# Kernel tuning notes

Measured on AMD Instinct MI355X. Metric: run time of the kernel, lower is better.

The kernel has to match this reference:

```python
import jax, jax.numpy as jnp
import numpy as np

B, S, H, L = 64, 512, 768, 2
OP, C, M, E, A = 18, 24, 16, 8, 3
K = C + M + E          # 48 operand classes
PAD = 0                # label_pad_id


def _linear(x, W, b):
    return x @ W.T + b


def _ln(x, g, b):
    mu = x.mean(-1, keepdims=True)
    v = ((x - mu) ** 2).mean(-1, keepdims=True)
    return (x - mu) / jnp.sqrt(v + 1e-5) * g + b


def _proj(x, W, b, g, be):
    return _ln(_linear(x, W, b), g, be)


def _mlp(x, W1, b1, W2, b2):
    return _linear(jax.nn.relu(_linear(x, W1, b1)), W2, b2)


def _gru(x, hx, Wih, Whh, bih, bhh):
    # single time-step multi-layer GRU (torch nn.GRU gate math), x:[B,H], hx:[L,B,H]
    hs = []
    for l in range(L):
        gi = _linear(x, Wih[l], bih[l])
        gh = _linear(hx[l], Whh[l], bhh[l])
        ir, iz, inn = jnp.split(gi, 3, axis=-1)
        hr, hz, hn = jnp.split(gh, 3, axis=-1)
        r = jax.nn.sigmoid(ir + hr)
        z = jax.nn.sigmoid(iz + hz)
        n = jnp.tanh(inn + r * hn)
        x = (1.0 - z) * n + z * hx[l]
        hs.append(x)
    return x, jnp.stack(hs)


def _pick(idx, pc, pn, prev, bidx):
    # get_operand_vector: const -> projected const, number -> projected number, else previous result
    is_c = idx < C
    i2 = idx - C
    is_n = (i2 >= 0) & (i2 < M)
    i3 = i2 - M
    is_p = (i3 >= 0) & (i3 < E)
    v = jnp.where(is_c[:, None], pc[jnp.clip(idx, 0, C - 1)], 0.0)
    v = jnp.where(is_n[:, None], pn[bidx, jnp.clip(i2, 0, M - 1)], v)
    v = jnp.where(is_p[:, None], prev[bidx, jnp.clip(i3, 0, E - 1)], v)
    return v


def _forward(inp, const_vector, operator_vector, opj_W, opj_b, opj_g, opj_be, odj_W, odj_b, odj_g, odj_be, opc_W1, opc_b1, opc_W2, opc_b2, odc_W1, odc_b1, odc_W2, odc_b2, og_Wih, og_Whh, og_bih, og_bhh, cg_Wih, cg_Whh, cg_bih, cg_bhh, number_mask, gold_operators, gold_operands):
    Bv, Sv, Hv = inp.shape
    # _get_num_vec (concat=True): first/last token embedding per number id
    match = number_mask[:, :, None] == (jnp.arange(M) + 1)[None, None, :]   # [B,S,M]
    exists = match.any(axis=1)                                              # [B,M]
    first = jnp.argmax(match, axis=1)
    last = Sv - 1 - jnp.argmax(match[:, ::-1, :], axis=1)
    fv = jnp.take_along_axis(inp, first[..., None], axis=1)                 # [B,M,H]
    lv = jnp.take_along_axis(inp, last[..., None], axis=1)
    num_vec = jnp.where(exists[..., None], jnp.concatenate([fv, lv], -1), 0.0)  # [B,M,2H]
    pn = _proj(num_vec, odj_W, odj_b, odj_g, odj_be)                        # [B,M,H]
    pc = _proj(const_vector, odj_W, odj_b, odj_g, odj_be)                   # [C,H]
    gold_opv = _proj(operator_vector[gold_operators], opj_W, opj_b, opj_g, opj_be)  # [B,E,H]

    prev = jnp.zeros((Bv, E, Hv), inp.dtype)   # previous_result_vector
    bidx = jnp.arange(Bv)
    cv = inp[:, 0, :]
    ctx_hx = None
    op_logits, od_logits = [], []
    for i in range(E):
        if i > 0:
            cv, _ = _gru(cv, ctx_hx, cg_Wih, cg_Whh, cg_bih, cg_bhh)
        op_logits.append(_mlp(cv, opc_W1, opc_b1, opc_W2, opc_b2))
        hx = jnp.broadcast_to(cv, (L, Bv, Hv))
        step_logits = []
        pred = None
        for j in range(A):
            if j == 0:
                x = gold_opv[:, i]  # teacher forcing (module default training=True)
            else:
                x = _pick(gold_operands[:, i, j - 1], pc, pn, prev, bidx)
            x, hx = _gru(x, hx, og_Wih, og_Whh, og_bih, og_bhh)
            logit = _mlp(x, odc_W1, odc_b1, odc_W2, odc_b2)
            step_logits.append(logit)
            oidx = jnp.argmax(logit, axis=1)
            empty = jnp.max(prev[:, i, :], axis=-1) == 0
            cond = (oidx < C) & (oidx == PAD) & empty
            prev = prev.at[:, i].set(jnp.where(cond[:, None], x, prev[:, i]))
            pred = _pick(oidx, pc, pn, prev, bidx)
        empty = jnp.max(prev[:, i, :], axis=-1) == 0
        prev = prev.at[:, i].set(jnp.where(empty[:, None], pred, prev[:, i]))
        ctx_hx = jnp.broadcast_to(prev[:, i], (L, Bv, Hv))
        od_logits.append(jnp.stack(step_logits, axis=1))
    return jnp.stack(op_logits, axis=1), jnp.stack(od_logits, axis=1)


def setup_inputs() -> dict:
    key = jax.random.key(0)
    ks = iter(jax.random.split(key, 48))
    def rn(shape, s=0.02):
        return jax.random.normal(next(ks), shape, jnp.float32) * s
    d = {}
    d["input"] = jax.random.normal(next(ks), (B, S, H), jnp.float32)
    d["attention_mask"] = jax.random.randint(next(ks), (B, S), 0, 2, jnp.int32)
    d["question_mask"] = jax.random.randint(next(ks), (B, S), 0, 2, jnp.int32)
    d["number_mask"] = jax.random.randint(next(ks), (B, S), 0, M + 1, jnp.int32)
    d["gold_operators"] = jax.random.randint(next(ks), (B, E), 0, OP, jnp.int32)
    d["gold_operands"] = jax.random.randint(next(ks), (B, E, A), 0, K, jnp.int32)
    d["const_vector"] = rn((C, 2 * H), 1.0)
    d["operator_vector"] = rn((OP, 2 * H), 1.0)
    d["opj_W"] = rn((H, 2 * H)); d["opj_b"] = jnp.zeros(H); d["opj_g"] = jnp.ones(H); d["opj_be"] = jnp.zeros(H)
    d["odj_W"] = rn((H, 2 * H)); d["odj_b"] = jnp.zeros(H); d["odj_g"] = jnp.ones(H); d["odj_be"] = jnp.zeros(H)
    d["opc_W1"] = rn((H // 2, H)); d["opc_b1"] = jnp.zeros(H // 2)
    d["opc_W2"] = rn((OP, H // 2)); d["opc_b2"] = jnp.zeros(OP)
    d["odc_W1"] = rn((K // 2, H)); d["odc_b1"] = jnp.zeros(K // 2)
    d["odc_W2"] = rn((K, K // 2)); d["odc_b2"] = jnp.zeros(K)
    for p in ["og", "cg"]:
        d[p + "_Wih"] = rn((L, 3 * H, H)); d[p + "_Whh"] = rn((L, 3 * H, H))
        d[p + "_bih"] = jnp.zeros((L, 3 * H)); d[p + "_bhh"] = jnp.zeros((L, 3 * H))
    return d


def reference(input, attention_mask, question_mask, number_mask, gold_operators, gold_operands, const_vector, operator_vector, opj_W, opj_b, opj_g, opj_be, odj_W, odj_b, odj_g, odj_be, opc_W1, opc_b1, opc_W2, opc_b2, odc_W1, odc_b1, odc_W2, odc_b2, og_Wih, og_Whh, og_bih, og_bhh, cg_Wih, cg_Whh, cg_bih, cg_bhh):
    # attention_mask / question_mask are unused by the original forward as well
    return _forward(input, const_vector, operator_vector, opj_W, opj_b, opj_g, opj_be, odj_W, odj_b, odj_g, odj_be, opc_W1, opc_b1, opc_W2, opc_b2, odc_W1, odc_b1, odc_W2, odc_b2, og_Wih, og_Whh, og_bih, og_bhh, cg_Wih, cg_Whh, cg_bih, cg_bhh, number_mask, gold_operators, gold_operands)
```

## Files before the change

kernel.cpp:

```cpp
#include <hip/hip_runtime.h>
#include <math.h>

constexpr int B_  = 64;
constexpr int S_  = 512;
constexpr int H_  = 768;
constexpr int H2_ = 1536;
constexpr int G3_ = 2304;
constexpr int OP_ = 18;
constexpr int C_  = 24;
constexpr int M_  = 16;
constexpr int E_  = 8;
constexpr int A_  = 3;
constexpr int K_  = 48;
constexpr int HH_ = 384;

using f32x4  = __attribute__((ext_vector_type(4))) float;
using short8 = __attribute__((ext_vector_type(8))) short;

#define MFMA16(a, b, c) __builtin_amdgcn_mfma_f32_16x16x32_bf16((a), (b), (c), 0, 0, 0)

__device__ __forceinline__ void split1(float x, short& h, short& l)
{
    union { float f; unsigned u; } a; a.f = x;
    h = (short)(a.u >> 16);
    union { unsigned u; float f; } hb; hb.u = a.u & 0xffff0000u;
    union { float f; unsigned u; } r; r.f = x - hb.f;
    l = (short)(r.u >> 16);
}

__device__ __forceinline__ void cvt8(float4 p0, float4 p1, short8& hi, short8& lo)
{
    float x[8] = {p0.x, p0.y, p0.z, p0.w, p1.x, p1.y, p1.z, p1.w};
    #pragma unroll
    for (int e = 0; e < 8; ++e) { short h, l; split1(x[e], h, l); hi[e] = h; lo[e] = l; }
}

__global__ void k_split_all(
    const float* __restrict__ s0, short* __restrict__ h0, short* __restrict__ l0, int e0,
    const float* __restrict__ s1, short* __restrict__ h1, short* __restrict__ l1, int e1,
    const float* __restrict__ s2, short* __restrict__ h2, short* __restrict__ l2, int e2,
    const float* __restrict__ s3, short* __restrict__ h3, short* __restrict__ l3, int e3,
    const float* __restrict__ s4, short* __restrict__ h4, short* __restrict__ l4, int e4,
    const float* __restrict__ s5, short* __restrict__ h5, short* __restrict__ l5, int e5)
{
    int t = blockIdx.x * 256 + threadIdx.x;
    if (t >= e5) return;
    const float* src; short* hi; short* lo; int base;
    if      (t < e0) { src = s0; hi = h0; lo = l0; base = 0;  }
    else if (t < e1) { src = s1; hi = h1; lo = l1; base = e0; }
    else if (t < e2) { src = s2; hi = h2; lo = l2; base = e1; }
    else if (t < e3) { src = s3; hi = h3; lo = l3; base = e2; }
    else if (t < e4) { src = s4; hi = h4; lo = l4; base = e3; }
    else             { src = s5; hi = h5; lo = l5; base = e4; }
    int u = t - base;
    float4 v = ((const float4*)src)[u];
    float x[4] = {v.x, v.y, v.z, v.w};
    short h[4], l[4];
    #pragma unroll
    for (int e = 0; e < 4; ++e) split1(x[e], h[e], l[e]);
    ((short4*)hi)[u] = make_short4(h[0], h[1], h[2], h[3]);
    ((short4*)lo)[u] = make_short4(l[0], l[1], l[2], l[3]);
}

__global__ __launch_bounds__(512) void k_gru_mfma(
    int ghonly,
    const short* __restrict__ xhi, const short* __restrict__ xlo, long ldx, int pickmode,
    const int* __restrict__ gopd, int i, int jm1,
    const short* __restrict__ pchi, const short* __restrict__ pclo,
    const short* __restrict__ pnhi, const short* __restrict__ pnlo,
    const short* __restrict__ pvhi, const short* __restrict__ pvlo,
    const short* __restrict__ hhi, const short* __restrict__ hlo, long ldh,
    const short* __restrict__ Wih_hi, const short* __restrict__ Wih_lo,
    const short* __restrict__ Whh_hi, const short* __restrict__ Whh_lo,
    float* __restrict__ C)
{
    const int tid  = threadIdx.x;
    const int lane = tid & 63;
    const int w    = tid >> 6;
    const int bx   = blockIdx.x;
    const bool hside = ghonly || (bx >= 72);
    const int n0 = ((hside && !ghonly) ? bx - 72 : bx) * 32;
    const int koff = (lane >> 4) * 8;

    const short* ahi[4]; const short* alo[4];
    #pragma unroll
    for (int rt = 0; rt < 4; ++rt) {
        int r = rt * 16 + (lane & 15);
        long off;
        const short *bh_, *bl_;
        if (hside) { bh_ = hhi; bl_ = hlo; off = (long)r * ldh; }
        else if (!pickmode) { bh_ = xhi; bl_ = xlo; off = (long)r * ldx; }
        else {
            int idx = gopd[(r * E_ + i) * A_ + jm1];
            if (idx < C_)           { bh_ = pchi; bl_ = pclo; off = (long)idx * H_; }
            else if (idx < C_ + M_) { bh_ = pnhi; bl_ = pnlo; off = ((long)r * M_ + (idx - C_)) * H_; }
            else                    { bh_ = pvhi; bl_ = pvlo; off = ((long)r * E_ + (idx - C_ - M_)) * H_; }
        }
        ahi[rt] = bh_ + off + koff;
        alo[rt] = bl_ + off + koff;
    }
    const short* whi[2]; const short* wlo[2];
    const short* WH = hside ? Whh_hi : Wih_hi;
    const short* WL = hside ? Whh_lo : Wih_lo;
    #pragma unroll
    for (int nt = 0; nt < 2; ++nt) {
        long off = (long)(n0 + nt * 16 + (lane & 15)) * H_ + koff;
        whi[nt] = WH + off;
        wlo[nt] = WL + off;
    }

    f32x4 acc[4][2];
    #pragma unroll
    for (int rt = 0; rt < 4; ++rt)
        #pragma unroll
        for (int nt = 0; nt < 2; ++nt) acc[rt][nt] = (f32x4){0.f, 0.f, 0.f, 0.f};

    for (int kt = w * 3; kt < w * 3 + 3; ++kt) {
        const int kb = kt * 32;
        short8 Ah[4], Al[4];
        #pragma unroll
        for (int rt = 0; rt < 4; ++rt) {
            Ah[rt] = *(const short8*)(ahi[rt] + kb);
            Al[rt] = *(const short8*)(alo[rt] + kb);
        }
        #pragma unroll
        for (int nt = 0; nt < 2; ++nt) {
            short8 Bh = *(const short8*)(whi[nt] + kb);
            short8 Bl = *(const short8*)(wlo[nt] + kb);
            #pragma unroll
            for (int rt = 0; rt < 4; ++rt) {
                acc[rt][nt] = MFMA16(Ah[rt], Bh, acc[rt][nt]);
                acc[rt][nt] = MFMA16(Ah[rt], Bl, acc[rt][nt]);
                acc[rt][nt] = MFMA16(Al[rt], Bh, acc[rt][nt]);
            }
        }
    }

    __shared__ f32x4 Lr[8][8][64];
    #pragma unroll
    for (int rt = 0; rt < 4; ++rt)
        #pragma unroll
        for (int nt = 0; nt < 2; ++nt)
            Lr[w][rt * 2 + nt][lane] = acc[rt][nt];
    __syncthreads();
    {
        const int f  = w;
        const int rt = f >> 1, nt = f & 1;
        f32x4 s = Lr[0][f][lane];
        #pragma unroll
        for (int q = 1; q < 8; ++q) s = s + Lr[q][f][lane];
        float* Cb = C + (hside ? 2304 : 0) + n0;
        int col = nt * 16 + (lane & 15);
        int rb  = rt * 16 + ((lane >> 4) << 2);
        #pragma unroll
        for (int r = 0; r < 4; ++r)
            Cb[(long)(rb + r) * 4608 + col] = s[r];
    }
}

__global__ __launch_bounds__(512) void k_gi_pre(
    const short* __restrict__ xhi, const short* __restrict__ xlo,
    const short* __restrict__ Whi, const short* __restrict__ Wlo,
    float* __restrict__ C)
{
    const int tid  = threadIdx.x;
    const int lane = tid & 63;
    const int w    = tid >> 6;
    const int n0 = blockIdx.x * 32;
    const int r0 = blockIdx.y * 64;
    const int koff = (lane >> 4) * 8;

    const short* ahi[4]; const short* alo[4];
    #pragma unroll
    for (int rt = 0; rt < 4; ++rt) {
        long off = (long)(r0 + rt * 16 + (lane & 15)) * H_ + koff;
        ahi[rt] = xhi + off;
        alo[rt] = xlo + off;
    }
    const short* whi[2]; const short* wlo[2];
    #pragma unroll
    for (int nt = 0; nt < 2; ++nt) {
        long off = (long)(n0 + nt * 16 + (lane & 15)) * H_ + koff;
        whi[nt] = Whi + off;
        wlo[nt] = Wlo + off;
    }

    f32x4 acc[4][2];
    #pragma unroll
    for (int rt = 0; rt < 4; ++rt)
        #pragma unroll
        for (int nt = 0; nt < 2; ++nt) acc[rt][nt] = (f32x4){0.f, 0.f, 0.f, 0.f};

    for (int kt = w * 3; kt < w * 3 + 3; ++kt) {
        const int kb = kt * 32;
        short8 Ah[4], Al[4];
        #pragma unroll
        for (int rt = 0; rt < 4; ++rt) {
            Ah[rt] = *(const short8*)(ahi[rt] + kb);
            Al[rt] = *(const short8*)(alo[rt] + kb);
        }
        #pragma unroll
        for (int nt = 0; nt < 2; ++nt) {
            short8 Bh = *(const short8*)(whi[nt] + kb);
            short8 Bl = *(const short8*)(wlo[nt] + kb);
            #pragma unroll
            for (int rt = 0; rt < 4; ++rt) {
                acc[rt][nt] = MFMA16(Ah[rt], Bh, acc[rt][nt]);
                acc[rt][nt] = MFMA16(Ah[rt], Bl, acc[rt][nt]);
                acc[rt][nt] = MFMA16(Al[rt], Bh, acc[rt][nt]);
            }
        }
    }

    __shared__ f32x4 Lr[8][8][64];
    #pragma unroll
    for (int rt = 0; rt < 4; ++rt)
        #pragma unroll
        for (int nt = 0; nt < 2; ++nt)
            Lr[w][rt * 2 + nt][lane] = acc[rt][nt];
    __syncthreads();
    {
        const int f  = w;
        const int rt = f >> 1, nt = f & 1;
        f32x4 s = Lr[0][f][lane];
        #pragma unroll
        for (int q = 1; q < 8; ++q) s = s + Lr[q][f][lane];
        int col = n0 + nt * 16 + (lane & 15);
        int rb  = r0 + rt * 16 + ((lane >> 4) << 2);
        #pragma unroll
        for (int r = 0; r < 4; ++r)
            C[(long)(rb + r) * G3_ + col] = s[r];
    }
}

__global__ __launch_bounds__(512) void k_proj_mfma(
    const float* __restrict__ Ab, long lda, const int* __restrict__ gidx, int Mm,
    const short* __restrict__ Whi, const short* __restrict__ Wlo, int wld,
    float* __restrict__ C, int ldc)
{
    const int tid  = threadIdx.x;
    const int lane = tid & 63;
    const int w    = tid >> 6;
    const int n0 = blockIdx.x * 64;
    const int r0 = blockIdx.y * 64;
    const int koff = (lane >> 4) * 8;

    const float* arow[4];
    #pragma unroll
    for (int rt = 0; rt < 4; ++rt) {
        int r = r0 + rt * 16 + (lane & 15);
        int rr = r < Mm ? r : (Mm - 1);
        const float* s = gidx ? (Ab + (long)gidx[rr] * lda) : (Ab + (long)rr * lda);
        arow[rt] = s + koff;
    }
    const short* whi[4]; const short* wlo[4];
    #pragma unroll
    for (int nt = 0; nt < 4; ++nt) {
        long off = (long)(n0 + nt * 16 + (lane & 15)) * wld + koff;
        whi[nt] = Whi + off; wlo[nt] = Wlo + off;
    }

    f32x4 acc[4][4];
    #pragma unroll
    for (int rt = 0; rt < 4; ++rt)
        #pragma unroll
        for (int nt = 0; nt < 4; ++nt) acc[rt][nt] = (f32x4){0.f, 0.f, 0.f, 0.f};

    for (int kt = w * 6; kt < w * 6 + 6; ++kt) {
        const int kb = kt * 32;
        short8 ah[4], al[4];
        #pragma unroll
        for (int rt = 0; rt < 4; ++rt) {
            float4 p0 = *(const float4*)(arow[rt] + kb);
            float4 p1 = *(const float4*)(arow[rt] + kb + 4);
            cvt8(p0, p1, ah[rt], al[rt]);
        }
        #pragma unroll
        for (int nt = 0; nt < 4; ++nt) {
            short8 Bh = *(const short8*)(whi[nt] + kb);
            short8 Bl = *(const short8*)(wlo[nt] + kb);
            #pragma unroll
            for (int rt = 0; rt < 4; ++rt) {
                acc[rt][nt] = MFMA16(ah[rt], Bh, acc[rt][nt]);
                acc[rt][nt] = MFMA16(ah[rt], Bl, acc[rt][nt]);
                acc[rt][nt] = MFMA16(al[rt], Bh, acc[rt][nt]);
            }
        }
    }

    __shared__ f32x4 Lr[112][64];
    if (w > 0) {
        #pragma unroll
        for (int rt = 0; rt < 4; ++rt)
            #pragma unroll
            for (int nt = 0; nt < 4; ++nt)
                Lr[(w - 1) * 16 + rt * 4 + nt][lane] = acc[rt][nt];
    }
    __syncthreads();
    if (w == 0) {
        #pragma unroll
        for (int rt = 0; rt < 4; ++rt)
            #pragma unroll
            for (int nt = 0; nt < 4; ++nt) {
                int f = rt * 4 + nt;
                f32x4 s = acc[rt][nt];
                #pragma unroll
                for (int q = 0; q < 7; ++q) s = s + Lr[q * 16 + f][lane];
                int col = n0 + nt * 16 + (lane & 15);
                int rb  = r0 + rt * 16 + ((lane >> 4) << 2);
                #pragma unroll
                for (int r = 0; r < 4; ++r)
                    if (rb + r < Mm) C[(long)(rb + r) * ldc + col] = s[r];
            }
    }
}

__global__ void k_gates2(const float* __restrict__ GI, long ldgi,
                         const float* __restrict__ GH, long ldgh,
                         const float* __restrict__ h, long ldh,
                         const float* __restrict__ bih, const float* __restrict__ bhh,
                         float* __restrict__ hnew,
                         short* __restrict__ hnhi, short* __restrict__ hnlo)
{
    int t = blockIdx.x * 256 + threadIdx.x;
    int b = t / 768, c = t - b * 768;
    const float* gi = GI + (long)b * ldgi;
    const float* gh = GH + (long)b * ldgh;
    float ir  = gi[c]        + bih[c];
    float iz  = gi[768 + c]  + bih[768 + c];
    float in_ = gi[1536 + c] + bih[1536 + c];
    float hr  = gh[c]        + bhh[c];
    float hz  = gh[768 + c]  + bhh[768 + c];
    float hn  = gh[1536 + c] + bhh[1536 + c];
    float r  = 1.f / (1.f + expf(-(ir + hr)));
    float z_ = 1.f / (1.f + expf(-(iz + hz)));
    float n  = tanhf(in_ + r * hn);
    float hp = h[(long)b * ldh + c];
    float v = (1.f - z_) * n + z_ * hp;
    hnew[t] = v;
    short sh, sl; split1(v, sh, sl);
    hnhi[t] = sh; hnlo[t] = sl;
}

__global__ void k_ln2(float* __restrict__ X, const float* __restrict__ bias,
                      const float* __restrict__ g, const float* __restrict__ be,
                      short* __restrict__ Xhi, short* __restrict__ Xlo)
{
    int row = blockIdx.x, tid = threadIdx.x;
    __shared__ float red[256];
    float* xr = X + (long)row * 768;
    float v[3];
    #pragma unroll
    for (int it = 0; it < 3; ++it) {
        int c2 = tid + it * 256;
        v[it] = xr[c2] + bias[c2];
    }
    float s = v[0] + v[1] + v[2];
    red[tid] = s; __syncthreads();
    for (int o = 128; o > 0; o >>= 1) { if (tid < o) red[tid] += red[tid + o]; __syncthreads(); }
    float mu = red[0] / 768.f;
    __syncthreads();
    float vv = 0.f;
    #pragma unroll
    for (int it = 0; it < 3; ++it) { float d = v[it] - mu; vv += d * d; }
    red[tid] = vv; __syncthreads();
    for (int o = 128; o > 0; o >>= 1) { if (tid < o) red[tid] += red[tid + o]; __syncthreads(); }
    float inv = 1.f / sqrtf(red[0] / 768.f + 1e-5f);
    #pragma unroll
    for (int it = 0; it < 3; ++it) {
        int c2 = tid + it * 256;
        float o2 = (v[it] - mu) * inv * g[c2] + be[c2];
        xr[c2] = o2;
        short sh, sl; split1(o2, sh, sl);
        Xhi[(long)row * 768 + c2] = sh;
        Xlo[(long)row * 768 + c2] = sl;
    }
}

__global__ __launch_bounds__(256) void k_ophead_fused(
    int do_gates,
    const float* __restrict__ GI,
    const float* __restrict__ bihg, const float* __restrict__ bhhg,
    const float* __restrict__ hp, long ldhp,
    float* __restrict__ cvf, short* __restrict__ cvhi, short* __restrict__ cvlo,
    const float* __restrict__ W1, const float* __restrict__ b1,
    const float* __restrict__ W2, const float* __restrict__ b2,
    float* __restrict__ op_out, int i)
{
    int b = blockIdx.x, tid = threadIdx.x;
    __shared__ float xs[768];
    __shared__ float hs[384];

    if (do_gates) {
        const float* gb = GI + (long)b * 4608;
        #pragma unroll
        for (int it = 0; it < 3; ++it) {
            int c2 = tid + it * 256;
            float ir  = gb[c2]        + bihg[c2];
            float iz  = gb[768 + c2]  + bihg[768 + c2];
            float in_ = gb[1536 + c2] + bihg[1536 + c2];
            float hr  = gb[2304 + c2] + bhhg[c2];
            float hz  = gb[3072 + c2] + bhhg[768 + c2];
            float hn  = gb[3840 + c2] + bhhg[1536 + c2];
            float r  = 1.f / (1.f + expf(-(ir + hr)));
            float z_ = 1.f / (1.f + expf(-(iz + hz)));
            float n  = tanhf(in_ + r * hn);
            float hpv = hp[(long)b * ldhp + c2];
            float v = (1.f - z_) * n + z_ * hpv;
            xs[c2] = v;
            cvf[(long)b * 768 + c2] = v;
            short sh, sl; split1(v, sh, sl);
            cvhi[(long)b * 768 + c2] = sh;
            cvlo[(long)b * 768 + c2] = sl;
        }
    } else {
        const float* xr = cvf + (long)b * 768;
        #pragma unroll
        for (int it = 0; it < 3; ++it) xs[tid + it * 256] = xr[tid + it * 256];
    }
    __syncthreads();

    for (int c = tid; c < 384; c += 256) {
        const float* wr = W1 + (long)c * 768;
        float acc = 0.f;
        #pragma unroll 8
        for (int k = 0; k < 768; k += 4) {
            float4 xv = *(const float4*)&xs[k];
            float4 wv = *(const float4*)(wr + k);
            acc += xv.x * wv.x + xv.y * wv.y + xv.z * wv.z + xv.w * wv.w;
        }
        hs[c] = fmaxf(acc + b1[c], 0.f);
    }
    __syncthreads();

    int c = tid >> 3, g = tid & 7;
    float acc = 0.f;
    if (c < OP_) {
        const float* wr = W2 + (long)c * HH_;
        #pragma unroll
        for (int t = 0; t < 12; ++t) {
            int k = (g + 8 * t) * 4;
            float4 xv = *(const float4*)&hs[k];
            float4 wv = *(const float4*)(wr + k);
            acc += xv.x * wv.x + xv.y * wv.y + xv.z * wv.z + xv.w * wv.w;
        }
    }
    acc += __shfl_xor(acc, 1);
    acc += __shfl_xor(acc, 2);
    acc += __shfl_xor(acc, 4);
    if (c < OP_ && g == 0)
        op_out[((long)b * E_ + i) * OP_ + c] = acc + b2[c];
}

__global__ __launch_bounds__(256) void k_odhead(
    const float* __restrict__ GI,
    const float* __restrict__ bihg, const float* __restrict__ bhhg,
    const float* __restrict__ hp, long ldhp,
    float* __restrict__ hx1f, short* __restrict__ hx1hi, short* __restrict__ hx1lo,
    const float* __restrict__ W1, const float* __restrict__ b1,
    const float* __restrict__ W2, const float* __restrict__ b2,
    float* __restrict__ od_base, long ldl,
    float* __restrict__ prev, int i,
    const float* __restrict__ pcb, const float* __restrict__ pnb,
    short* __restrict__ pvhi, short* __restrict__ pvlo,
    int do_final)
{
    int b = blockIdx.x, tid = threadIdx.x;
    __shared__ float xs[768];
    __shared__ float ps[768];
    __shared__ float hidL[24];
    __shared__ float lg[48];
    __shared__ float red[256];
    __shared__ int s_oidx;

    {
        const float* gb = GI + (long)b * 4608;
        #pragma unroll
        for (int it = 0; it < 3; ++it) {
            int c2 = tid + it * 256;
            float ir  = gb[c2]        + bihg[c2];
            float iz  = gb[768 + c2]  + bihg[768 + c2];
            float in_ = gb[1536 + c2] + bihg[1536 + c2];
            float hr  = gb[2304 + c2] + bhhg[c2];
            float hz  = gb[3072 + c2] + bhhg[768 + c2];
            float hn  = gb[3840 + c2] + bhhg[1536 + c2];
            float r  = 1.f / (1.f + expf(-(ir + hr)));
            float z_ = 1.f / (1.f + expf(-(iz + hz)));
            float n  = tanhf(in_ + r * hn);
            float hpv = hp[(long)b * ldhp + c2];
            float v = (1.f - z_) * n + z_ * hpv;
            xs[c2] = v;
            hx1f[(long)b * 768 + c2] = v;
            short sh, sl; split1(v, sh, sl);
            hx1hi[(long)b * 768 + c2] = sh;
            hx1lo[(long)b * 768 + c2] = sl;
        }
    }
    __syncthreads();

    int c = tid >> 3, g = tid & 7;
    float acc = 0.f;
    if (c < 24) {
        const float* wr = W1 + (long)c * 768;
        #pragma unroll
        for (int t = 0; t < 24; ++t) {
            int k = (g + 8 * t) * 4;
            float4 xv = *(const float4*)&xs[k];
            float4 wv = *(const float4*)(wr + k);
            acc += xv.x * wv.x + xv.y * wv.y + xv.z * wv.z + xv.w * wv.w;
        }
    }
    acc += __shfl_xor(acc, 1);
    acc += __shfl_xor(acc, 2);
    acc += __shfl_xor(acc, 4);
    if (c < 24 && g == 0) hidL[c] = fmaxf(acc + b1[c], 0.f);
    __syncthreads();

    if (tid < 48) {
        float a2 = b2[tid];
        const float* w2 = W2 + tid * 24;
        #pragma unroll
        for (int k = 0; k < 24; ++k) a2 += hidL[k] * w2[k];
        lg[tid] = a2;
        od_base[(long)b * ldl + tid] = a2;
    }

    long poff = ((long)b * E_ + i) * 768;
    float* prow = prev + poff;
    float m = -3.4e38f;
    #pragma unroll
    for (int it = 0; it < 3; ++it) m = fmaxf(m, prow[tid + it * 256]);
    red[tid] = m; __syncthreads();
    for (int o = 128; o > 0; o >>= 1) { if (tid < o) red[tid] = fmaxf(red[tid], red[tid + o]); __syncthreads(); }
    float m0 = red[0];

    if (tid == 0) {
        float best = lg[0]; int bi = 0;
        for (int k2 = 1; k2 < K_; ++k2) { float v = lg[k2]; if (v > best) { best = v; bi = k2; } }
        s_oidx = bi;
    }
    __syncthreads();
    int oidx = s_oidx;
    bool empty0 = (m0 == 0.0f);
    bool cond = (oidx == 0) && empty0;
    if (cond) {
        #pragma unroll
        for (int it = 0; it < 3; ++it) {
            int c2 = tid + it * 256;
            float v = xs[c2];
            prow[c2] = v;
            short sh, sl; split1(v, sh, sl);
            pvhi[poff + c2] = sh; pvlo[poff + c2] = sl;
        }
    }
    __syncthreads();

    if (!do_final) return;

    float mfin;
    if (cond) {
        float mx = -3.4e38f;
        #pragma unroll
        for (int it = 0; it < 3; ++it) mx = fmaxf(mx, xs[tid + it * 256]);
        red[tid] = mx; __syncthreads();
        for (int o = 128; o > 0; o >>= 1) { if (tid < o) red[tid] = fmaxf(red[tid], red[tid + o]); __syncthreads(); }
        mfin = red[0];
    } else {
        mfin = m0;
    }

    const float* src;
    if (oidx < C_)            src = pcb + (long)oidx * 768;
    else if (oidx < C_ + M_)  src = pnb + ((long)b * M_ + (oidx - C_)) * 768;
    else                      src = prev + ((long)b * E_ + (oidx - C_ - M_)) * 768;
    #pragma unroll
    for (int it = 0; it < 3; ++it) ps[tid + it * 256] = src[tid + it * 256];
    __syncthreads();

    if (mfin == 0.0f) {
        #pragma unroll
        for (int it = 0; it < 3; ++it) {
            int c2 = tid + it * 256;
            float v = ps[c2];
            prow[c2] = v;
            short sh, sl; split1(v, sh, sl);
            pvhi[poff + c2] = sh; pvlo[poff + c2] = sl;
        }
    }
}

__global__ void k_numvec(const float* __restrict__ inp, const int* __restrict__ nmask,
                         float* __restrict__ numvec)
{
    int b = blockIdx.x / M_, m = blockIdx.x % M_;
    int tid = threadIdx.x;
    int fmin = S_, lmax = -1;
    for (int s = tid; s < S_; s += 256) {
        if (nmask[b * S_ + s] == m + 1) {
            if (s < fmin) fmin = s;
            if (s > lmax) lmax = s;
        }
    }
    __shared__ int sf[256], sl[256];
    sf[tid] = fmin; sl[tid] = lmax; __syncthreads();
    for (int o = 128; o > 0; o >>= 1) {
        if (tid < o) {
            sf[tid] = min(sf[tid], sf[tid + o]);
            sl[tid] = max(sl[tid], sl[tid + o]);
        }
        __syncthreads();
    }
    int first = sf[0], last = sl[0];
    bool exists = (last >= 0);
    if (!exists) { first = 0; last = 0; }
    const float* fv = inp + ((long)b * S_ + first) * H_;
    const float* lv = inp + ((long)b * S_ + last) * H_;
    float* dst = numvec + ((long)b * M_ + m) * H2_;
    for (int h = tid; h < H_; h += 256) {
        dst[h]      = exists ? fv[h] : 0.f;
        dst[H_ + h] = exists ? lv[h] : 0.f;
    }
}

__global__ void k_copy_cv(const float* __restrict__ inp, float* __restrict__ cvv,
                          short* __restrict__ cvhi, short* __restrict__ cvlo)
{
    int b = blockIdx.x;
    for (int h = threadIdx.x; h < H_; h += 256) {
        float v = inp[(long)b * S_ * H_ + h];
        cvv[b * H_ + h] = v;
        short sh, sl; split1(v, sh, sl);
        cvhi[b * H_ + h] = sh; cvlo[b * H_ + h] = sl;
    }
}

extern "C" void kernel_launch(void* const* d_in, const int* in_sizes, int n_in,
                              void* d_out, int out_size, void* d_ws, size_t ws_size,
                              hipStream_t stream)
{
    const float* inp    = (const float*)d_in[0];
    const int*   nmask  = (const int*)  d_in[3];
    const int*   gops   = (const int*)  d_in[4];
    const int*   gopd   = (const int*)  d_in[5];
    const float* constv = (const float*)d_in[6];
    const float* opv    = (const float*)d_in[7];
    const float* opj_W  = (const float*)d_in[8];
    const float* opj_b  = (const float*)d_in[9];
    const float* opj_g  = (const float*)d_in[10];
    const float* opj_be = (const float*)d_in[11];
    const float* odj_W  = (const float*)d_in[12];
    const float* odj_b  = (const float*)d_in[13];
    const float* odj_g  = (const float*)d_in[14];
    const float* odj_be = (const float*)d_in[15];
    const float* opc_W1 = (const float*)d_in[16];
    const float* opc_b1 = (const float*)d_in[17];
    const float* opc_W2 = (const float*)d_in[18];
    const float* opc_b2 = (const float*)d_in[19];
    const float* odc_W1 = (const float*)d_in[20];
    const float* odc_b1 = (const float*)d_in[21];
    const float* odc_W2 = (const float*)d_in[22];
    const float* odc_b2 = (const float*)d_in[23];
    const float* og_Wih = (const float*)d_in[24];
    const float* og_Whh = (const float*)d_in[25];
    const float* og_bih = (const float*)d_in[26];
    const float* og_bhh = (const float*)d_in[27];
    const float* cg_Wih = (const float*)d_in[28];
    const float* cg_Whh = (const float*)d_in[29];
    const float* cg_bih = (const float*)d_in[30];
    const float* cg_bhh = (const float*)d_in[31];

    float* op_out = (float*)d_out;
    float* od_out = op_out + (long)B_ * E_ * OP_;

    float* ws      = (float*)d_ws;
    float* num_vec = ws; ws += (long)B_ * M_ * H2_;
    float* pn      = ws; ws += (long)B_ * M_ * H_;
    float* pcb     = ws; ws += (long)64 * H_;
    float* gopv    = ws; ws += (long)B_ * E_ * H_;
    float* prev    = ws; ws += (long)B_ * E_ * H_;
    float* gigh    = ws; ws += (long)B_ * 4608;
    float* gi_pre  = ws; ws += (long)B_ * E_ * G3_;
    float* cv      = ws; ws += (long)B_ * H_;
    float* h0      = ws; ws += (long)B_ * H_;
    float* hx0     = ws; ws += (long)B_ * H_;
    float* hx1     = ws; ws += (long)B_ * H_;

    auto alloc_s = [&](long elems) -> short* {
        short* p = (short*)ws; ws += elems / 2; return p;
    };
    const long nOG = (long)2 * G3_ * H_;
    short* og_ih_hi = alloc_s(nOG); short* og_ih_lo = alloc_s(nOG);
    short* og_hh_hi = alloc_s(nOG); short* og_hh_lo = alloc_s(nOG);
    short* cg_ih_hi = alloc_s(nOG); short* cg_ih_lo = alloc_s(nOG);
    short* cg_hh_hi = alloc_s(nOG); short* cg_hh_lo = alloc_s(nOG);
    const long nPJ = (long)H_ * H2_;
    short* odj_hi = alloc_s(nPJ); short* odj_lo = alloc_s(nPJ);
    short* opj_hi = alloc_s(nPJ); short* opj_lo = alloc_s(nPJ);
    short* pn_hi  = alloc_s((long)B_ * M_ * H_); short* pn_lo  = alloc_s((long)B_ * M_ * H_);
    short* pc_hi  = alloc_s((long)64 * H_);      short* pc_lo  = alloc_s((long)64 * H_);
    short* gv_hi  = alloc_s((long)B_ * E_ * H_); short* gv_lo  = alloc_s((long)B_ * E_ * H_);
    short* pv_hi  = alloc_s((long)B_ * E_ * H_); short* pv_lo  = alloc_s((long)B_ * E_ * H_);
    short* cv_hi  = alloc_s((long)B_ * H_);      short* cv_lo  = alloc_s((long)B_ * H_);
    short* h0_hi  = alloc_s((long)B_ * H_);      short* h0_lo  = alloc_s((long)B_ * H_);
    short* hx0_hi = alloc_s((long)B_ * H_);      short* hx0_lo = alloc_s((long)B_ * H_);
    short* hx1_hi = alloc_s((long)B_ * H_);      short* hx1_lo = alloc_s((long)B_ * H_);

    hipMemsetAsync(prev, 0, (size_t)B_ * E_ * H_ * sizeof(float), stream);
    hipMemsetAsync(pv_hi, 0, (size_t)2 * B_ * E_ * H_ * sizeof(short), stream);

    {
        int nOG4 = (int)(nOG / 4), nPJ4 = (int)(nPJ / 4);
        int e0 = nOG4, e1 = 2 * nOG4, e2 = 3 * nOG4, e3 = 4 * nOG4;
        int e4 = e3 + nPJ4, e5 = e4 + nPJ4;
        k_split_all<<<(e5 + 255) / 256, 256, 0, stream>>>(
            og_Wih, og_ih_hi, og_ih_lo, e0,
            og_Whh, og_hh_hi, og_hh_lo, e1,
            cg_Wih, cg_ih_hi, cg_ih_lo, e2,
            cg_Whh, cg_hh_hi, cg_hh_lo, e3,
            odj_W,  odj_hi,  odj_lo,  e4,
            opj_W,  opj_hi,  opj_lo,  e5);
    }

    k_numvec<<<B_ * M_, 256, 0, stream>>>(inp, nmask, num_vec);

    k_proj_mfma<<<dim3(12, 16), 512, 0, stream>>>(num_vec, H2_, nullptr, 1024,
                                                  odj_hi, odj_lo, H2_, pn, H_);
    k_ln2<<<1024, 256, 0, stream>>>(pn, odj_b, odj_g, odj_be, pn_hi, pn_lo);

    k_proj_mfma<<<dim3(12, 1), 512, 0, stream>>>(constv, H2_, nullptr, C_,
                                                 odj_hi, odj_lo, H2_, pcb, H_);
    k_ln2<<<C_, 256, 0, stream>>>(pcb, odj_b, odj_g, odj_be, pc_hi, pc_lo);

    k_proj_mfma<<<dim3(12, 8), 512, 0, stream>>>(opv, H2_, gops, 512,
                                                 opj_hi, opj_lo, H2_, gopv, H_);
    k_ln2<<<512, 256, 0, stream>>>(gopv, opj_b, opj_g, opj_be, gv_hi, gv_lo);

    k_gi_pre<<<dim3(72, 8), 512, 0, stream>>>(gv_hi, gv_lo, og_ih_hi, og_ih_lo, gi_pre);

    k_copy_cv<<<B_, 256, 0, stream>>>(inp, cv, cv_hi, cv_lo);

    const long ldE = (long)E_ * H_;
    const long lW  = (long)G3_ * H_;

    for (int i = 0; i < E_; ++i) {
        if (i > 0) {
            const float* hrow = prev + (long)(i - 1) * H_;
            const short* hrhi = pv_hi + (long)(i - 1) * H_;
            const short* hrlo = pv_lo + (long)(i - 1) * H_;
            k_gru_mfma<<<144, 512, 0, stream>>>(0, cv_hi, cv_lo, H_, 0, nullptr, 0, 0,
                                                nullptr, nullptr, nullptr, nullptr, nullptr, nullptr,
                                                hrhi, hrlo, ldE,
                                                cg_ih_hi, cg_ih_lo, cg_hh_hi, cg_hh_lo, gigh);
            k_gates2<<<192, 256, 0, stream>>>(gigh, 4608, gigh + 2304, 4608,
                                              hrow, ldE, cg_bih, cg_bhh, h0, h0_hi, h0_lo);
            k_gru_mfma<<<144, 512, 0, stream>>>(0, h0_hi, h0_lo, H_, 0, nullptr, 0, 0,
                                                nullptr, nullptr, nullptr, nullptr, nullptr, nullptr,
                                                hrhi, hrlo, ldE,
                                                cg_ih_hi + lW, cg_ih_lo + lW,
                                                cg_hh_hi + lW, cg_hh_lo + lW, gigh);
            k_ophead_fused<<<B_, 256, 0, stream>>>(1, gigh, cg_bih + G3_, cg_bhh + G3_,
                                                   hrow, ldE, cv, cv_hi, cv_lo,
                                                   opc_W1, opc_b1, opc_W2, opc_b2, op_out, i);
        } else {
            k_ophead_fused<<<B_, 256, 0, stream>>>(0, gigh, cg_bih, cg_bhh,
                                                   cv, H_, cv, cv_hi, cv_lo,
                                                   opc_W1, opc_b1, opc_W2, opc_b2, op_out, i);
        }

        for (int j = 0; j < A_; ++j) {
            const float* hp0 = (j == 0) ? cv : hx0;
            const float* hp1 = (j == 0) ? cv : hx1;
            const short* hp0hi = (j == 0) ? cv_hi : hx0_hi;
            const short* hp0lo = (j == 0) ? cv_lo : hx0_lo;
            const short* hp1hi = (j == 0) ? cv_hi : hx1_hi;
            const short* hp1lo = (j == 0) ? cv_lo : hx1_lo;

            if (j == 0) {
                k_gru_mfma<<<72, 512, 0, stream>>>(1, nullptr, nullptr, 0, 0, nullptr, 0, 0,
                                                   nullptr, nullptr, nullptr, nullptr, nullptr, nullptr,
                                                   hp0hi, hp0lo, H_,
                                                   og_ih_hi, og_ih_lo, og_hh_hi, og_hh_lo, gigh);
                k_gates2<<<192, 256, 0, stream>>>(gi_pre + (long)i * G3_, (long)E_ * G3_,
                                                  gigh + 2304, 4608,
                                                  hp0, H_, og_bih, og_bhh, hx0, hx0_hi, hx0_lo);
            } else {
                k_gru_mfma<<<144, 512, 0, stream>>>(0, nullptr, nullptr, 0, 1, gopd, i, j - 1,
                                                    pc_hi, pc_lo, pn_hi, pn_lo, pv_hi, pv_lo,
                                                    hp0hi, hp0lo, H_,
                                                    og_ih_hi, og_ih_lo, og_hh_hi, og_hh_lo, gigh);
                k_gates2<<<192, 256, 0, stream>>>(gigh, 4608, gigh + 2304, 4608,
                                                  hp0, H_, og_bih, og_bhh, hx0, hx0_hi, hx0_lo);
            }
            k_gru_mfma<<<144, 512, 0, stream>>>(0, hx0_hi, hx0_lo, H_, 0, nullptr, 0, 0,
                                                nullptr, nullptr, nullptr, nullptr, nullptr, nullptr,
                                                hp1hi, hp1lo, H_,
                                                og_ih_hi + lW, og_ih_lo + lW,
                                                og_hh_hi + lW, og_hh_lo + lW, gigh);

            float* od_base = od_out + ((long)i * A_ + j) * K_;
            k_odhead<<<B_, 256, 0, stream>>>(gigh, og_bih + G3_, og_bhh + G3_,
                                             hp1, H_, hx1, hx1_hi, hx1_lo,
                                             odc_W1, odc_b1, odc_W2, odc_b2,
                                             od_base, (long)E_ * A_ * K_,
                                             prev, i, pcb, pn, pv_hi, pv_lo,
                                             (j == A_ - 1) ? 1 : 0);
        }
    }
}
```

Baseline: 1.395 ms.

## Split GRU GEMM K dimension across two blocks with partial sums reduced in consumers

The per-step GRU matvec kernel now uses 256-thread blocks and a second grid dimension that splits the K=768 reduction in half. Each half writes its partials to a separate slab of the doubled gigh buffer. The gate kernels (k_gates2, ophead, odhead) add the two partials before applying the biases. This doubles the number of blocks to fill more of the GPU's compute units on these small latency-bound launches. The cost is extra global writes and reads of the partial sums and a slightly different float summation order.

Result: no change. 1.413 ms (+1.3%).

```diff
diff --git a/kernel.cpp b/kernel.cpp
--- a/kernel.cpp
+++ b/kernel.cpp
@@ -13,6 +13,7 @@
 constexpr int A_  = 3;
 constexpr int K_  = 48;
 constexpr int HH_ = 384;
+constexpr long HOFF = 294912;
 
 using f32x4  = __attribute__((ext_vector_type(4))) float;
 using short8 = __attribute__((ext_vector_type(8))) short;
@@ -62,7 +63,7 @@
     ((short4*)lo)[u] = make_short4(l[0], l[1], l[2], l[3]);
 }
 
-__global__ __launch_bounds__(512) void k_gru_mfma(
+__global__ __launch_bounds__(256) void k_gru_mfma(
     int ghonly,
     const short* __restrict__ xhi, const short* __restrict__ xlo, long ldx, int pickmode,
     const int* __restrict__ gopd, int i, int jm1,
@@ -78,6 +79,7 @@
     const int lane = tid & 63;
     const int w    = tid >> 6;
     const int bx   = blockIdx.x;
+    const int kz   = blockIdx.y;
     const bool hside = ghonly || (bx >= 72);
     const int n0 = ((hside && !ghonly) ? bx - 72 : bx) * 32;
     const int koff = (lane >> 4) * 8;
@@ -115,7 +117,8 @@
         #pragma unroll
         for (int nt = 0; nt < 2; ++nt) acc[rt][nt] = (f32x4){0.f, 0.f, 0.f, 0.f};
 
-    for (int kt = w * 3; kt < w * 3 + 3; ++kt) {
+    const int kt0 = kz * 12 + w * 3;
+    for (int kt = kt0; kt < kt0 + 3; ++kt) {
         const int kb = kt * 32;
         short8 Ah[4], Al[4];
         #pragma unroll
@@ -136,20 +139,21 @@
         }
     }
 
-    __shared__ f32x4 Lr[8][8][64];
+    __shared__ f32x4 Lr[4][8][64];
     #pragma unroll
     for (int rt = 0; rt < 4; ++rt)
         #pragma unroll
         for (int nt = 0; nt < 2; ++nt)
             Lr[w][rt * 2 + nt][lane] = acc[rt][nt];
     __syncthreads();
-    {
-        const int f  = w;
+    #pragma unroll
+    for (int ff = 0; ff < 2; ++ff) {
+        const int f  = w * 2 + ff;
         const int rt = f >> 1, nt = f & 1;
         f32x4 s = Lr[0][f][lane];
         #pragma unroll
-        for (int q = 1; q < 8; ++q) s = s + Lr[q][f][lane];
-        float* Cb = C + (hside ? 2304 : 0) + n0;
+        for (int q = 1; q < 4; ++q) s = s + Lr[q][f][lane];
+        float* Cb = C + (long)kz * HOFF + (hside ? 2304 : 0) + n0;
         int col = nt * 16 + (lane & 15);
         int rb  = rt * 16 + ((lane >> 4) << 2);
         #pragma unroll
@@ -315,8 +319,8 @@
     }
 }
 
-__global__ void k_gates2(const float* __restrict__ GI, long ldgi,
-                         const float* __restrict__ GH, long ldgh,
+__global__ void k_gates2(const float* __restrict__ GI, long ldgi, long gi2off,
+                         const float* __restrict__ GH, long ldgh, long gh2off,
                          const float* __restrict__ h, long ldh,
                          const float* __restrict__ bih, const float* __restrict__ bhh,
                          float* __restrict__ hnew,
@@ -326,12 +330,24 @@
     int b = t / 768, c = t - b * 768;
     const float* gi = GI + (long)b * ldgi;
     const float* gh = GH + (long)b * ldgh;
-    float ir  = gi[c]        + bih[c];
-    float iz  = gi[768 + c]  + bih[768 + c];
-    float in_ = gi[1536 + c] + bih[1536 + c];
-    float hr  = gh[c]        + bhh[c];
-    float hz  = gh[768 + c]  + bhh[768 + c];
-    float hn  = gh[1536 + c] + bhh[1536 + c];
+    float ir  = gi[c];
+    float iz  = gi[768 + c];
+    float in_ = gi[1536 + c];
+    if (gi2off) {
+        ir  += gi[gi2off + c];
+        iz  += gi[gi2off + 768 + c];
+        in_ += gi[gi2off + 1536 + c];
+    }
+    float hr  = gh[c];
+    float hz  = gh[768 + c];
+    float hn  = gh[1536 + c];
+    if (gh2off) {
+        hr  += gh[gh2off + c];
+        hz  += gh[gh2off + 768 + c];
+        hn  += gh[gh2off + 1536 + c];
+    }
+    ir += bih[c]; iz += bih[768 + c]; in_ += bih[1536 + c];
+    hr += bhh[c]; hz += bhh[768 + c]; hn  += bhh[1536 + c];
     float r  = 1.f / (1.f + expf(-(ir + hr)));
     float z_ = 1.f / (1.f + expf(-(iz + hz)));
     float n  = tanhf(in_ + r * hn);
@@ -392,16 +408,17 @@
     __shared__ float hs[384];
 
     if (do_gates) {
-        const float* gb = GI + (long)b * 4608;
+        const float* gb  = GI + (long)b * 4608;
+        const float* gb2 = gb + HOFF;
         #pragma unroll
         for (int it = 0; it < 3; ++it) {
             int c2 = tid + it * 256;
-            float ir  = gb[c2]        + bihg[c2];
-            float iz  = gb[768 + c2]  + bihg[768 + c2];
-            float in_ = gb[1536 + c2] + bihg[1536 + c2];
-            float hr  = gb[2304 + c2] + bhhg[c2];
-            float hz  = gb[3072 + c2] + bhhg[768 + c2];
-            float hn  = gb[3840 + c2] + bhhg[1536 + c2];
+            float ir  = (gb[c2]        + gb2[c2])        + bihg[c2];
+            float iz  = (gb[768 + c2]  + gb2[768 + c2])  + bihg[768 + c2];
+            float in_ = (gb[1536 + c2] + gb2[1536 + c2]) + bihg[1536 + c2];
+            float hr  = (gb[2304 + c2] + gb2[2304 + c2]) + bhhg[c2];
+            float hz  = (gb[3072 + c2] + gb2[3072 + c2]) + bhhg[768 + c2];
+            float hn  = (gb[3840 + c2] + gb2[3840 + c2]) + bhhg[1536 + c2];
             float r  = 1.f / (1.f + expf(-(ir + hr)));
             float z_ = 1.f / (1.f + expf(-(iz + hz)));
             float n  = tanhf(in_ + r * hn);
@@ -474,16 +491,17 @@
     __shared__ int s_oidx;
 
     {
-        const float* gb = GI + (long)b * 4608;
+        const float* gb  = GI + (long)b * 4608;
+        const float* gb2 = gb + HOFF;
         #pragma unroll
         for (int it = 0; it < 3; ++it) {
             int c2 = tid + it * 256;
-            float ir  = gb[c2]        + bihg[c2];
-            float iz  = gb[768 + c2]  + bihg[768 + c2];
-            float in_ = gb[1536 + c2] + bihg[1536 + c2];
-            float hr  = gb[2304 + c2] + bhhg[c2];
-            float hz  = gb[3072 + c2] + bhhg[768 + c2];
-            float hn  = gb[3840 + c2] + bhhg[1536 + c2];
+            float ir  = (gb[c2]        + gb2[c2])        + bihg[c2];
+            float iz  = (gb[768 + c2]  + gb2[768 + c2])  + bihg[768 + c2];
+            float in_ = (gb[1536 + c2] + gb2[1536 + c2]) + bihg[1536 + c2];
+            float hr  = (gb[2304 + c2] + gb2[2304 + c2]) + bhhg[c2];
+            float hz  = (gb[3072 + c2] + gb2[3072 + c2]) + bhhg[768 + c2];
+            float hn  = (gb[3840 + c2] + gb2[3840 + c2]) + bhhg[1536 + c2];
             float r  = 1.f / (1.f + expf(-(ir + hr)));
             float z_ = 1.f / (1.f + expf(-(iz + hz)));
             float n  = tanhf(in_ + r * hn);
@@ -678,7 +696,7 @@
     float* pcb     = ws; ws += (long)64 * H_;
     float* gopv    = ws; ws += (long)B_ * E_ * H_;
     float* prev    = ws; ws += (long)B_ * E_ * H_;
-    float* gigh    = ws; ws += (long)B_ * 4608;
+    float* gigh    = ws; ws += (long)2 * B_ * 4608;
     float* gi_pre  = ws; ws += (long)B_ * E_ * G3_;
     float* cv      = ws; ws += (long)B_ * H_;
     float* h0      = ws; ws += (long)B_ * H_;
@@ -747,13 +765,13 @@
             const float* hrow = prev + (long)(i - 1) * H_;
             const short* hrhi = pv_hi + (long)(i - 1) * H_;
             const short* hrlo = pv_lo + (long)(i - 1) * H_;
-            k_gru_mfma<<<144, 512, 0, stream>>>(0, cv_hi, cv_lo, H_, 0, nullptr, 0, 0,
+            k_gru_mfma<<<dim3(144, 2), 256, 0, stream>>>(0, cv_hi, cv_lo, H_, 0, nullptr, 0, 0,
                                                 nullptr, nullptr, nullptr, nullptr, nullptr, nullptr,
                                                 hrhi, hrlo, ldE,
                                                 cg_ih_hi, cg_ih_lo, cg_hh_hi, cg_hh_lo, gigh);
-            k_gates2<<<192, 256, 0, stream>>>(gigh, 4608, gigh + 2304, 4608,
+            k_gates2<<<192, 256, 0, stream>>>(gigh, 4608, HOFF, gigh + 2304, 4608, HOFF,
                                               hrow, ldE, cg_bih, cg_bhh, h0, h0_hi, h0_lo);
-            k_gru_mfma<<<144, 512, 0, stream>>>(0, h0_hi, h0_lo, H_, 0, nullptr, 0, 0,
+            k_gru_mfma<<<dim3(144, 2), 256, 0, stream>>>(0, h0_hi, h0_lo, H_, 0, nullptr, 0, 0,
                                                 nullptr, nullptr, nullptr, nullptr, nullptr, nullptr,
                                                 hrhi, hrlo, ldE,
                                                 cg_ih_hi + lW, cg_ih_lo + lW,
@@ -776,22 +794,22 @@
             const short* hp1lo = (j == 0) ? cv_lo : hx1_lo;
 
             if (j == 0) {
-                k_gru_mfma<<<72, 512, 0, stream>>>(1, nullptr, nullptr, 0, 0, nullptr, 0, 0,
+                k_gru_mfma<<<dim3(72, 2), 256, 0, stream>>>(1, nullptr, nullptr, 0, 0, nullptr, 0, 0,
                                                    nullptr, nullptr, nullptr, nullptr, nullptr, nullptr,
                                                    hp0hi, hp0lo, H_,
                                                    og_ih_hi, og_ih_lo, og_hh_hi, og_hh_lo, gigh);
-                k_gates2<<<192, 256, 0, stream>>>(gi_pre + (long)i * G3_, (long)E_ * G3_,
-                                                  gigh + 2304, 4608,
+                k_gates2<<<192, 256, 0, stream>>>(gi_pre + (long)i * G3_, (long)E_ * G3_, 0,
+                                                  gigh + 2304, 4608, HOFF,
                                                   hp0, H_, og_bih, og_bhh, hx0, hx0_hi, hx0_lo);
             } else {
-                k_gru_mfma<<<144, 512, 0, stream>>>(0, nullptr, nullptr, 0, 1, gopd, i, j - 1,
+                k_gru_mfma<<<dim3(144, 2), 256, 0, stream>>>(0, nullptr, nullptr, 0, 1, gopd, i, j - 1,
                                                     pc_hi, pc_lo, pn_hi, pn_lo, pv_hi, pv_lo,
                                                     hp0hi, hp0lo, H_,
                                                     og_ih_hi, og_ih_lo, og_hh_hi, og_hh_lo, gigh);
-                k_gates2<<<192, 256, 0, stream>>>(gigh, 4608, gigh + 2304, 4608,
+                k_gates2<<<192, 256, 0, stream>>>(gigh, 4608, HOFF, gigh + 2304, 4608, HOFF,
                                                   hp0, H_, og_bih, og_bhh, hx0, hx0_hi, hx0_lo);
             }
-            k_gru_mfma<<<144, 512, 0, stream>>>(0, hx0_hi, hx0_lo, H_, 0, nullptr, 0, 0,
+            k_gru_mfma<<<dim3(144, 2), 256, 0, stream>>>(0, hx0_hi, hx0_lo, H_, 0, nullptr, 0, 0,
                                                 nullptr, nullptr, nullptr, nullptr, nullptr, nullptr,
                                                 hp1hi, hp1lo, H_,
                                                 og_ih_hi + lW, og_ih_lo + lW,
```
